# Kernel tuning notes

Measured on AMD Instinct MI355X. Metric: run time of the kernel, lower is better.

Reference implementation:

```python
import jax, jax.numpy as jnp
import numpy as np

N, B, E, D, DQ, H = 20000, 32, 320000, 128, 1024, 2
L = N // B  # 625 nodes per graph (equal-size graphs -> static max_node_num)
NUM_GNN_LAYERS = 3


def setup_inputs() -> dict:
    key = jax.random.key(0)
    ks = jax.random.split(key, 32)
    rn = lambda k, s, scale=1.0: jax.random.normal(k, s, jnp.float32) * scale
    w = lambda k, fi, fo: rn(k, (fi, fo), 1.0 / np.sqrt(fi))
    inp = {
        'x': rn(ks[0], (N, D)),
        'edge_attr': rn(ks[1], (E, D)),
        'u': rn(ks[2], (B, D)),
        'qa_attr': rn(ks[3], (B, DQ)),
        # edge MLP: cat(src,dest,edge_attr,u[eb]) = 4D -> hidden D -> D
        'W_e1': w(ks[4], 4 * D, D), 'b_e1': jnp.zeros((D,)),
        'W_e2': w(ks[5], D, D), 'b_e2': jnp.zeros((D,)),
        # weight mlp: cat(edge_attr, u[eb]) = 2D -> 1 (num_layers=1)
        'W_w': w(ks[6], 2 * D, 1), 'b_w': jnp.zeros((1,)),
        # message mlp: cat(x[row], edge_attr) = 2D -> D -> D
        'W_m1': w(ks[7], 2 * D, D), 'b_m1': jnp.zeros((D,)),
        'W_m2': w(ks[8], D, D), 'b_m2': jnp.zeros((D,)),
        # update mlp: cat(x, received, u[nb]) = 3D -> D -> D
        'W_u1': w(ks[9], 3 * D, D), 'b_u1': jnp.zeros((D,)),
        'W_u2': w(ks[10], D, D), 'b_u2': jnp.zeros((D,)),
        # multihead att-pool: q from qa_attr (DQ) -> H*dk; k,v from evidence (D) -> H*dk
        'W_q': w(ks[11], DQ, D), 'b_q': jnp.zeros((D,)),
        'W_k': w(ks[12], D, D), 'b_k': jnp.zeros((D,)),
        'W_v': w(ks[13], D, D), 'b_v': jnp.zeros((D,)),
        'edge_index': jax.random.randint(ks[14], (2, E), 0, N, dtype=jnp.int32),
        'node_batch': (jnp.arange(N, dtype=jnp.int32) // L).astype(jnp.int32),
        'num_of_nodes': jnp.full((B,), L, dtype=jnp.int32),
    }
    return inp


def _mlp2(h, W1, b1, W2, b2):
    return jax.nn.relu(h @ W1 + b1) @ W2 + b2


def _seg_softmax(logits, seg, num):
    m = jax.ops.segment_max(logits, seg, num_segments=num)
    e = jnp.exp(logits - m[seg])
    s = jax.ops.segment_sum(e, seg, num_segments=num)
    return e / s[seg]


def reference(x, edge_attr, u, qa_attr,
              W_e1, b_e1, W_e2, b_e2, W_w, b_w,
              W_m1, b_m1, W_m2, b_m2, W_u1, b_u1, W_u2, b_u2,
              W_q, b_q, W_k, b_k, W_v, b_v,
              edge_index, node_batch, num_of_nodes):
    row, col = edge_index[0], edge_index[1]
    edge_batch = node_batch[row]
    Bsz, Nn = u.shape[0], x.shape[0]
    Lm = Nn // Bsz  # static max_node_num (equal-size graphs)

    norm_w = None
    for _ in range(NUM_GNN_LAYERS):
        ue = u[edge_batch]  # [E, D]
        # EdgeModel: cat(src, dest, edge_attr, u[eb]) -> MLP -> new edge_attr
        new_edge = _mlp2(jnp.concatenate([x[row], x[col], edge_attr, ue], 1),
                         W_e1, b_e1, W_e2, b_e2)
        # edge weights from OLD edge_attr (per EdgeV1Model.forward)
        wts = jnp.concatenate([edge_attr, ue], 1) @ W_w + b_w  # [E,1]
        norm_w = _seg_softmax(wts[:, 0], edge_batch, Bsz)[:, None]  # [E,1]
        edge_attr = new_edge
        # NodeModel: message MLP, weighted scatter_mean over col, update MLP
        msg = _mlp2(jnp.concatenate([x[row], edge_attr], 1), W_m1, b_m1, W_m2, b_m2)
        summed = jax.ops.segment_sum(msg * norm_w, col, num_segments=Nn)
        cnt = jax.ops.segment_sum(jnp.ones((msg.shape[0],), msg.dtype), col, num_segments=Nn)
        received = summed / jnp.maximum(cnt, 1.0)[:, None]
        x = _mlp2(jnp.concatenate([x, received, u[node_batch]], 1),
                  W_u1, b_u1, W_u2, b_u2)

    pooled_edge = jax.ops.segment_sum(edge_attr * norm_w, edge_batch, num_segments=Bsz)  # [B,D]
    # evidence packing: equal graphs -> simple reshape, then exact GELU
    evidence = jax.nn.gelu(x.reshape(Bsz, Lm, -1), approximate=False)  # [B,L,D]
    mask = jnp.arange(Lm)[None, :] >= num_of_nodes[:, None]  # [B,L] True = masked

    # MultiheadAttPoolLayer
    dk = W_k.shape[1] // H
    q = (qa_attr @ W_q + b_q).reshape(Bsz, H, dk)
    k = (evidence @ W_k + b_k).reshape(Bsz, Lm, H, dk)
    v = (evidence @ W_v + b_v).reshape(Bsz, Lm, H, dk)
    scores = jnp.einsum('bhd,blhd->bhl', q, k) / jnp.sqrt(jnp.float32(dk))
    scores = jnp.where(mask[:, None, :], -1e30, scores)
    attn = jax.nn.softmax(scores, axis=-1)
    pooled_node = jnp.einsum('bhl,blhd->bhd', attn, v).reshape(Bsz, H * dk)  # [B,D]

    return jnp.concatenate([pooled_edge, pooled_node], 1)  # [B, 2D]
```

## Files before the change

### kernel.cpp

```cpp
#include <hip/hip_runtime.h>
#include <math.h>

typedef __bf16 bf16_t;
typedef bf16_t bf16x8 __attribute__((ext_vector_type(8)));
typedef bf16_t bf16x4 __attribute__((ext_vector_type(4)));
typedef float  f32x4  __attribute__((ext_vector_type(4)));

#define N_NODES 20000
#define NEDGE   320000
#define DIM     128
#define TP      136
#define EBLK    2500
#define FBLK    10000
#define NBLK    625

#define FE1  0
#define FE2  49152
#define FM1  65536
#define FM2  98304
#define FU1  114688
#define FU2  163840
#define FK   180224
#define FV   196608
#define WF_ELEMS 212992

__device__ __forceinline__ void acc_zero(f32x4 acc[2][8]) {
  f32x4 z = {0.f, 0.f, 0.f, 0.f};
#pragma unroll
  for (int i = 0; i < 2; ++i)
#pragma unroll
    for (int j = 0; j < 8; ++j) acc[i][j] = z;
}

__device__ __forceinline__ void wstage_rows_bf(bf16_t* sA, const bf16_t* src, int rowreg, int lane) {
  int r = lane >> 1, h = lane & 1;
  int row = __shfl(rowreg, r);
  const bf16_t* sp = src + (size_t)row * DIM + h * 64;
  bf16_t* dp = sA + r * TP + h * 64;
#pragma unroll
  for (int i = 0; i < 8; ++i)
    *(uint4*)(dp + i * 8) = *(const uint4*)(sp + i * 8);
}

__device__ __forceinline__ void wstage_rows_f32(bf16_t* sA, const float* src, int rowreg, int lane) {
  int r = lane >> 1, h = lane & 1;
  int row = __shfl(rowreg, r);
  const float* sp = src + (size_t)row * DIM + h * 64;
  bf16_t* dp = sA + r * TP + h * 64;
#pragma unroll
  for (int i = 0; i < 8; ++i) {
    float4 f0 = *(const float4*)(sp + i * 8);
    float4 f1 = *(const float4*)(sp + i * 8 + 4);
    bf16x8 tv;
    tv[0]=(bf16_t)f0.x; tv[1]=(bf16_t)f0.y; tv[2]=(bf16_t)f0.z; tv[3]=(bf16_t)f0.w;
    tv[4]=(bf16_t)f1.x; tv[5]=(bf16_t)f1.y; tv[6]=(bf16_t)f1.z; tv[7]=(bf16_t)f1.w;
    *(bf16x8*)(dp + i * 8) = tv;
  }
}

__device__ __forceinline__ void wstage_seq_bf(bf16_t* sA, const bf16_t* src, int base, int lane) {
  int r = lane >> 1, h = lane & 1;
  const bf16_t* sp = src + (size_t)(base + r) * DIM + h * 64;
  bf16_t* dp = sA + r * TP + h * 64;
#pragma unroll
  for (int i = 0; i < 8; ++i)
    *(uint4*)(dp + i * 8) = *(const uint4*)(sp + i * 8);
}

__device__ __forceinline__ void wstage_seq_f32(bf16_t* sA, const float* src, int base, int lane) {
  int r = lane >> 1, h = lane & 1;
  const float* sp = src + (size_t)(base + r) * DIM + h * 64;
  bf16_t* dp = sA + r * TP + h * 64;
#pragma unroll
  for (int i = 0; i < 8; ++i) {
    float4 f0 = *(const float4*)(sp + i * 8);
    float4 f1 = *(const float4*)(sp + i * 8 + 4);
    bf16x8 tv;
    tv[0]=(bf16_t)f0.x; tv[1]=(bf16_t)f0.y; tv[2]=(bf16_t)f0.z; tv[3]=(bf16_t)f0.w;
    tv[4]=(bf16_t)f1.x; tv[5]=(bf16_t)f1.y; tv[6]=(bf16_t)f1.z; tv[7]=(bf16_t)f1.w;
    *(bf16x8*)(dp + i * 8) = tv;
  }
}

__device__ __forceinline__ void wmfma_gk128(const bf16_t* sA, const bf16_t* __restrict__ Wf,
                                            int lane, int lm, int lq, f32x4 acc[2][8]) {
#pragma unroll
  for (int kk = 0; kk < 4; ++kk) {
    int ko = kk * 32 + lq * 8;
    bf16x8 a0 = *(const bf16x8*)(sA + lm * TP + ko);
    bf16x8 a1 = *(const bf16x8*)(sA + (16 + lm) * TP + ko);
    const bf16_t* wp = Wf + ((kk * 8) << 9) + (lane << 3);
#pragma unroll
    for (int ct = 0; ct < 8; ++ct) {
      bf16x8 bfr = *(const bf16x8*)(wp + (ct << 9));
      acc[0][ct] = __builtin_amdgcn_mfma_f32_16x16x32_bf16(a0, bfr, acc[0][ct], 0, 0, 0);
      acc[1][ct] = __builtin_amdgcn_mfma_f32_16x16x32_bf16(a1, bfr, acc[1][ct], 0, 0, 0);
    }
  }
}

__device__ __forceinline__ void merge_shfl(float& m, float& s, int width) {
  for (int k = 1; k < width; k <<= 1) {
    float m2 = __shfl_xor(m, k), s2 = __shfl_xor(s, k);
    float M = fmaxf(m, m2), ns = 0.f;
    if (m  > -1e29f) ns += s  * expf(m  - M);
    if (m2 > -1e29f) ns += s2 * expf(m2 - M);
    m = M; s = ns;
  }
}

__global__ void gn_xcvt(const float* x, bf16_t* xb) {
  int i = blockIdx.x * 256 + threadIdx.x;
  if (i < N_NODES * DIM / 4) {
    float4 f = ((const float4*)x)[i];
    bf16x4 o; o[0]=(bf16_t)f.x; o[1]=(bf16_t)f.y; o[2]=(bf16_t)f.z; o[3]=(bf16_t)f.w;
    *(bf16x4*)(xb + (size_t)i * 4) = o;
  }
}

__global__ void gn_fragw(const float* We1, const float* We2, const float* Wm1, const float* Wm2,
                         const float* Wu1, const float* Wu2, const float* Wk, const float* Wv,
                         bf16_t* WF) {
  int idx = blockIdx.x * 256 + threadIdx.x;
  if (idx >= WF_ELEMS) return;
  int seg = idx >> 14;
  const float* W; int kc;
  switch (seg) {
    case 0:  W = We1; kc = 0; break;
    case 1:  W = We1; kc = 1; break;
    case 2:  W = We1; kc = 2; break;
    case 3:  W = We2; kc = 0; break;
    case 4:  W = Wm1; kc = 0; break;
    case 5:  W = Wm1; kc = 1; break;
    case 6:  W = Wm2; kc = 0; break;
    case 7:  W = Wu1; kc = 0; break;
    case 8:  W = Wu1; kc = 1; break;
    case 9:  W = Wu1; kc = 2; break;
    case 10: W = Wu2; kc = 0; break;
    case 11: W = Wk;  kc = 0; break;
    default: W = Wv;  kc = 0; break;
  }
  int r = idx & 16383;
  int j = r & 7, lane = (r >> 3) & 63, ct = (r >> 9) & 7, kk = (r >> 12) & 3;
  int k = kc * 128 + kk * 32 + (lane >> 4) * 8 + j;
  int n = ct * 16 + (lane & 15);
  WF[idx] = (bf16_t)W[k * 128 + n];
}

__global__ void gn_uprep(const float* u, const float* We1, const float* be1,
// ... 34 lines not shown
  int t = threadIdx.x;
  int sub = t & 15, grp = t >> 4;
  for (int e = blockIdx.x * 16 + grp; e < NEDGE; e += gridDim.x * 16) {
    const float* er = ea + (size_t)e * DIM + sub * 8;
    float s = 0.f;
#pragma unroll
    for (int j = 0; j < 8; ++j) s += er[j] * Ww[sub * 8 + j];
#pragma unroll
    for (int m = 1; m < 16; m <<= 1) s += __shfl_xor(s, m);
    if (sub == 0) {
      int g = nbat[ei[e]];
      wl[e] = s + uw[g];
      gb[e] = g;
    }
  }
}

__global__ void gn_part0(const float* wl, const int* gb, float* pm, float* ps) {
  __shared__ float lv[128];
  __shared__ int   lgg[128];
  int t = threadIdx.x, blk = blockIdx.x, e0 = blk * 128;
  if (t < 128) { lv[t] = wl[e0 + t]; lgg[t] = gb[e0 + t]; }
  __syncthreads();
  int g = t >> 3, seg = t & 7;
  float m = -1e30f, s = 0.f;
  for (int i = seg * 16; i < seg * 16 + 16; ++i)
    if (lgg[i] == g) {
      float v = lv[i];
      if (v > m) { s = s * expf(m - v) + 1.f; m = v; }
      else s += expf(v - m);
    }
  merge_shfl(m, s, 8);
  if (seg == 0) { pm[blk * 32 + g] = m; ps[blk * 32 + g] = s; }
}

__global__ void gn_reduce_ms(const float* pm, const float* ps, float* mg, float* sg, int nb) {
  int g = blockIdx.x, t = threadIdx.x;
  __shared__ float red[256];
  float m = -1e30f;
  for (int i = t; i < nb; i += 256) m = fmaxf(m, pm[i * 32 + g]);
  red[t] = m; __syncthreads();
  for (int s2 = 128; s2 > 0; s2 >>= 1) { if (t < s2) red[t] = fmaxf(red[t], red[t + s2]); __syncthreads(); }
  m = red[0]; __syncthreads();
  float s = 0.f;
  for (int i = t; i < nb; i += 256) {
    float sb = ps[i * 32 + g];
    if (sb > 0.f) s += sb * expf(pm[i * 32 + g] - m);
  }
  red[t] = s; __syncthreads();
  for (int s2 = 128; s2 > 0; s2 >>= 1) { if (t < s2) red[t] += red[t + s2]; __syncthreads(); }
  if (t == 0) { mg[g] = m; sg[g] = red[0]; }
}

__global__ __launch_bounds__(64, 2) void gn_fused(
    const bf16_t* __restrict__ xb,
    const void* esrcv, int efirst,
    bf16_t* edst,
    const bf16_t* __restrict__ WF,
    const float* R, const float* UW, const float* Wwv,
    const float* be2, const float* bm1, const float* bm2,
    const float* wl_cur, const float* mg, const float* sg,
    float* wl_next, float* pm, float* ps, int last,
    const int* ei, const int* gb, float* recv) {
  __shared__ bf16_t sA[32 * TP];
  __shared__ float slwt[32];

  int lane = threadIdx.x;
  int blk = blockIdx.x;
  int e0 = blk * 32;
  int lm = lane & 15, lq = lane >> 4;

  int lrowr = 0, lcolr = 0, lgr = 0;
  float lnwr = 0.f;
  if (lane < 32) {
    int e = e0 + lane;
    lrowr = ei[e];
    lcolr = ei[NEDGE + e];
    int g = gb[e];
    lgr = g;
    lnwr = expf(wl_cur[e] - mg[g]) / sg[g];
  }

  f32x4 accE[2][8], accM[2][8];
  acc_zero(accE);
  acc_zero(accM);

  wstage_rows_bf(sA, xb, lrowr, lane);
  wmfma_gk128(sA, WF + FE1, lane, lm, lq, accE);
  wmfma_gk128(sA, WF + FM1, lane, lm, lq, accM);
  wstage_rows_bf(sA, xb, lcolr, lane);
  wmfma_gk128(sA, WF + FE1 + 16384, lane, lm, lq, accE);
  if (efirst) wstage_seq_f32(sA, (const float*)esrcv, e0, lane);
  else        wstage_seq_bf (sA, (const bf16_t*)esrcv, e0, lane);
  wmfma_gk128(sA, WF + FE1 + 32768, lane, lm, lq, accE);

#pragma unroll
  for (int rt = 0; rt < 2; ++rt)
#pragma unroll
    for (int reg = 0; reg < 4; ++reg) {
      int row = rt * 16 + lq * 4 + reg;
      const float* Rr = R + (size_t)__shfl(lgr, row) * DIM;
#pragma unroll
      for (int ct = 0; ct < 8; ++ct) {
        int col = ct * 16 + lm;
        sA[row * TP + col] = (bf16_t)fmaxf(accE[rt][ct][reg] + Rr[col], 0.f);
      }
    }
  acc_zero(accE);
  wmfma_gk128(sA, WF + FE2, lane, lm, lq, accE);

  {
    float ww8[8], be8[8];
#pragma unroll
    for (int ct = 0; ct < 8; ++ct) { ww8[ct] = Wwv[ct * 16 + lm]; be8[ct] = be2[ct * 16 + lm]; }
#pragma unroll
    for (int rt = 0; rt < 2; ++rt)
#pragma unroll
      for (int reg = 0; reg < 4; ++reg) {
        int row = rt * 16 + lq * 4 + reg;
        int g = __shfl(lgr, row);
        bf16_t* drow = edst + (size_t)(e0 + row) * DIM;
        float lsum = 0.f;
#pragma unroll
        for (int ct = 0; ct < 8; ++ct) {
          int col = ct * 16 + lm;
          float v = accE[rt][ct][reg] + be8[ct];
          drow[col] = (bf16_t)v;
          sA[row * TP + col] = (bf16_t)v;
          lsum += v * ww8[ct];
        }
        if (!last) {
          lsum += __shfl_xor(lsum, 1);
          lsum += __shfl_xor(lsum, 2);
          lsum += __shfl_xor(lsum, 4);
          lsum += __shfl_xor(lsum, 8);
          if (lm == 0) {
            float v2 = lsum + UW[g];
            wl_next[e0 + row] = v2;
            slwt[row] = v2;
          }
        }
      }
  }
  wmfma_gk128(sA, WF + FM1 + 16384, lane, lm, lq, accM);

  {
    float bm18[8];
#pragma unroll
    for (int ct = 0; ct < 8; ++ct) bm18[ct] = bm1[ct * 16 + lm];
#pragma unroll
    for (int rt = 0; rt < 2; ++rt)
#pragma unroll
      for (int reg = 0; reg < 4; ++reg) {
        int row = rt * 16 + lq * 4 + reg;
#pragma unroll
        for (int ct = 0; ct < 8; ++ct) {
          int col = ct * 16 + lm;
          sA[row * TP + col] = (bf16_t)fmaxf(accM[rt][ct][reg] + bm18[ct], 0.f);
        }
      }
  }
  acc_zero(accM);
  wmfma_gk128(sA, WF + FM2, lane, lm, lq, accM);

  {
    float bm28[8];
#pragma unroll
    for (int ct = 0; ct < 8; ++ct) bm28[ct] = bm2[ct * 16 + lm];
#pragma unroll
    for (int rt = 0; rt < 2; ++rt)
#pragma unroll
      for (int reg = 0; reg < 4; ++reg) {
        int row = rt * 16 + lq * 4 + reg;
        float nwv = __shfl(lnwr, row);
        float* rr = recv + (size_t)__shfl(lcolr, row) * DIM;
#pragma unroll
        for (int ct = 0; ct < 8; ++ct) {
          int col = ct * 16 + lm;
          atomicAdd(&rr[col], (accM[rt][ct][reg] + bm28[ct]) * nwv);
        }
      }
  }

  if (!last) {
    int g = lane >> 1, seg = lane & 1;
    float m = -1e30f, s = 0.f;
    for (int i = seg * 16; i < seg * 16 + 16; ++i) {
      int gi = __shfl(lgr, i);
      if (gi == g) {
        float v = slwt[i];
        if (v > m) { s = s * expf(m - v) + 1.f; m = v; }
        else s += expf(v - m);
      }
    }
    merge_shfl(m, s, 2);
    if (seg == 0) { pm[blk * 32 + g] = m; ps[blk * 32 + g] = s; }
  }
}

__global__ __launch_bounds__(64, 2) void gn_node(
    const bf16_t* xsrc, bf16_t* xdst, const float* recv, const float* cnt,
    const float* u, const bf16_t* __restrict__ WF,
    const float* bu1, const float* bu2, const int* nbat) {
  __shared__ bf16_t sA[32 * TP];

  int lane = threadIdx.x;
  int n0 = blockIdx.x * 32;
  int lm = lane & 15, lq = lane >> 4;

  int lgr = 0;
  if (lane < 32) lgr = nbat[n0 + lane];

  f32x4 acc[2][8];
  acc_zero(acc);

  wstage_seq_bf(sA, xsrc, n0, lane);
  wmfma_gk128(sA, WF + FU1, lane, lm, lq, acc);
  {
    int r = lane >> 1, h = lane & 1;
    const float* rr = recv + (size_t)(n0 + r) * DIM + h * 64;
    float ic = 1.f / fmaxf(cnt[n0 + r], 1.f);
    bf16_t* dp = sA + r * TP + h * 64;
#pragma unroll
    for (int i = 0; i < 8; ++i) {
      float4 f0 = *(const float4*)(rr + i * 8);
      float4 f1 = *(const float4*)(rr + i * 8 + 4);
      bf16x8 tv;
      tv[0]=(bf16_t)(f0.x*ic); tv[1]=(bf16_t)(f0.y*ic); tv[2]=(bf16_t)(f0.z*ic); tv[3]=(bf16_t)(f0.w*ic);
      tv[4]=(bf16_t)(f1.x*ic); tv[5]=(bf16_t)(f1.y*ic); tv[6]=(bf16_t)(f1.z*ic); tv[7]=(bf16_t)(f1.w*ic);
      *(bf16x8*)(dp + i * 8) = tv;
    }
  }
  wmfma_gk128(sA, WF + FU1 + 16384, lane, lm, lq, acc);
  wstage_rows_f32(sA, u, lgr, lane);
  wmfma_gk128(sA, WF + FU1 + 32768, lane, lm, lq, acc);

  {
    float bu18[8];
#pragma unroll
    for (int ct = 0; ct < 8; ++ct) bu18[ct] = bu1[ct * 16 + lm];
#pragma unroll
    for (int rt = 0; rt < 2; ++rt)
#pragma unroll
      for (int reg = 0; reg < 4; ++reg) {
        int row = rt * 16 + lq * 4 + reg;
#pragma unroll
        for (int ct = 0; ct < 8; ++ct) {
          int col = ct * 16 + lm;
          sA[row * TP + col] = (bf16_t)fmaxf(acc[rt][ct][reg] + bu18[ct], 0.f);
        }
      }
  }
  acc_zero(acc);
  wmfma_gk128(sA, WF + FU2, lane, lm, lq, acc);

  {
    float bu28[8];
#pragma unroll
    for (int ct = 0; ct < 8; ++ct) bu28[ct] = bu2[ct * 16 + lm];
#pragma unroll
    for (int rt = 0; rt < 2; ++rt)
#pragma unroll
      for (int reg = 0; reg < 4; ++reg) {
        int row = rt * 16 + lq * 4 + reg;
        bf16_t* dr = xdst + (size_t)(n0 + row) * DIM;
#pragma unroll
        for (int ct = 0; ct < 8; ++ct) {
          int col = ct * 16 + lm;
          dr[col] = (bf16_t)(acc[rt][ct][reg] + bu28[ct]);
        }
      }
  }
}

__global__ __launch_bounds__(64, 2) void gn_ev(
    const bf16_t* xsrc, const bf16_t* __restrict__ WF,
    const float* bk, const float* bv, float* kb, float* vb) {
  __shared__ bf16_t sA[32 * TP];

  int lane = threadIdx.x;
  int n0 = blockIdx.x * 32;
  int sel = blockIdx.y;
  const bf16_t* Wf = WF + (sel ? FV : FK);
  const float* bias = sel ? bv : bk;
  float* dst = sel ? vb : kb;
  int lm = lane & 15, lq = lane >> 4;

  {
    int r = lane >> 1, h = lane & 1;
    const bf16_t* sp = xsrc + (size_t)(n0 + r) * DIM + h * 64;
    bf16_t* dp = sA + r * TP + h * 64;
#pragma unroll
    for (int i = 0; i < 8; ++i) {
      uint4 v = *(const uint4*)(sp + i * 8);
      bf16_t tmp[8];
      *(uint4*)tmp = v;
      bf16x8 tv;
#pragma unroll
      for (int j = 0; j < 8; ++j) {
        float f = (float)tmp[j];
        tv[j] = (bf16_t)(0.5f * f * (1.f + erff(f * 0.70710678118654752f)));
      }
      *(bf16x8*)(dp + i * 8) = tv;
    }
  }

  f32x4 acc[2][8];
  acc_zero(acc);
  wmfma_gk128(sA, Wf, lane, lm, lq, acc);

  {
    float b8[8];
#pragma unroll
    for (int ct = 0; ct < 8; ++ct) b8[ct] = bias[ct * 16 + lm];
#pragma unroll
    for (int rt = 0; rt < 2; ++rt)
#pragma unroll
      for (int reg = 0; reg < 4; ++reg) {
        int row = rt * 16 + lq * 4 + reg;
        float* dr = dst + (size_t)(n0 + row) * DIM;
#pragma unroll
        for (int ct = 0; ct < 8; ++ct) {
          int col = ct * 16 + lm;
          dr[col] = acc[rt][ct][reg] + b8[ct];
        }
      }
  }
}

__global__ void gn_pooled_edge(const bf16_t* eb, const float* wl, const float* mg, const float* sg,
                               const int* gb, float* pe) {
  __shared__ float loc[4096];
  int t = threadIdx.x;
  for (int i = t; i < 4096; i += 256) loc[i] = 0.f;
  __syncthreads();
  int lane = t & 63, w = t >> 6;
  int wid = blockIdx.x * 4 + w, nw = gridDim.x * 4;
  for (int e = wid; e < NEDGE; e += nw) {
    int g = gb[e];
    float nwt = expf(wl[e] - mg[g]) / sg[g];
    const bf16_t* er = eb + (size_t)e * DIM + lane * 2;
    atomicAdd(&loc[g * 128 + lane * 2],     (float)er[0] * nwt);
    atomicAdd(&loc[g * 128 + lane * 2 + 1], (float)er[1] * nwt);
  }
  __syncthreads();
  for (int i = t; i < 4096; i += 256) atomicAdd(&pe[i], loc[i]);
}

__global__ void gn_att(const float* qb, const float* kb, const float* vb, const int* non, float* out) {
  int b = blockIdx.x >> 1, h = blockIdx.x & 1, t = threadIdx.x;
  __shared__ float qv[64];
  __shared__ float sc[625];
  __shared__ float red[256];
  if (t < 64) qv[t] = qb[b * 128 + h * 64 + t];
  __syncthreads();
  int nn = non[b];
  for (int l = t; l < 625; l += 256) {
    float acc = 0.f;
    const float* kr = kb + ((size_t)(b * 625 + l)) * DIM + h * 64;
    for (int d2 = 0; d2 < 64; ++d2) acc += qv[d2] * kr[d2];
    sc[l] = (l < nn) ? acc * 0.125f : -1e30f;
// ... 20 lines not shown
  }
}

__global__ void gn_fin(const float* pe, float* out) {
  int t = threadIdx.x;
  for (int i = t; i < 4096; i += 256) {
    int b = i >> 7, c = i & 127;
    out[b * 256 + c] = pe[i];
  }
}

extern "C" void kernel_launch(void* const* d_in, const int* in_sizes, int n_in,
                              void* d_out, int out_size, void* d_ws, size_t ws_size,
                              hipStream_t stream) {
  const float* x   = (const float*)d_in[0];
  const float* ea  = (const float*)d_in[1];
  const float* u   = (const float*)d_in[2];
  const float* qa  = (const float*)d_in[3];
  const float* We1 = (const float*)d_in[4];
  const float* be1 = (const float*)d_in[5];
  const float* We2 = (const float*)d_in[6];
  const float* be2 = (const float*)d_in[7];
  const float* Ww  = (const float*)d_in[8];
  const float* bw  = (const float*)d_in[9];
  const float* Wm1 = (const float*)d_in[10];
  const float* bm1 = (const float*)d_in[11];
  const float* Wm2 = (const float*)d_in[12];
  const float* bm2 = (const float*)d_in[13];
  const float* Wu1 = (const float*)d_in[14];
  const float* bu1 = (const float*)d_in[15];
  const float* Wu2 = (const float*)d_in[16];
  const float* bu2 = (const float*)d_in[17];
  const float* Wq  = (const float*)d_in[18];
  const float* bq  = (const float*)d_in[19];
  const float* Wk  = (const float*)d_in[20];
  const float* bk  = (const float*)d_in[21];
  const float* Wv  = (const float*)d_in[22];
  const float* bv  = (const float*)d_in[23];
  const int* ei   = (const int*)d_in[24];
  const int* nbat = (const int*)d_in[25];
  const int* non  = (const int*)d_in[26];
  float* out = (float*)d_out;

  char* p = (char*)d_ws;
  auto alloc = [&](size_t bytes) { char* r = p; p += (bytes + 255) & ~(size_t)255; return r; };
  bf16_t* EB  = (bf16_t*)alloc((size_t)NEDGE * DIM * 2);
  bf16_t* XB  = (bf16_t*)alloc((size_t)N_NODES * DIM * 2);
  bf16_t* XB0 = (bf16_t*)alloc((size_t)N_NODES * DIM * 2);
  float* RECV = (float*)alloc((size_t)N_NODES * DIM * 4);
  float* CNT  = (float*)alloc((size_t)N_NODES * 4);
  float* WL   = (float*)alloc((size_t)NEDGE * 4);
  float* WLn  = (float*)alloc((size_t)NEDGE * 4);
  int*   GB   = (int*)alloc((size_t)NEDGE * 4);
  float* PM   = (float*)alloc((size_t)FBLK * 32 * 4);
  float* PS   = (float*)alloc((size_t)FBLK * 32 * 4);
  float* MG   = (float*)alloc(32 * 4);
  float* SG   = (float*)alloc(32 * 4);
  float* R    = (float*)alloc(32 * 128 * 4);
  float* UW   = (float*)alloc(32 * 4);
  bf16_t* WF  = (bf16_t*)alloc((size_t)WF_ELEMS * 2);
  float* QB   = (float*)alloc(32 * 128 * 4);
  float* KB   = (float*)alloc((size_t)N_NODES * DIM * 4);
  float* VB   = (float*)alloc((size_t)N_NODES * DIM * 4);
  float* PE   = (float*)alloc(32 * 128 * 4);

  hipMemsetAsync(CNT, 0, (size_t)N_NODES * 4, stream);
  hipMemsetAsync(PE, 0, 32 * 128 * 4, stream);

  gn_xcvt<<<(N_NODES * DIM / 4 + 255) / 256, 256, 0, stream>>>(x, XB0);
  gn_fragw<<<(WF_ELEMS + 255) / 256, 256, 0, stream>>>(We1, We2, Wm1, Wm2, Wu1, Wu2, Wk, Wv, WF);
  gn_uprep<<<16, 256, 0, stream>>>(u, We1, be1, Ww, bw, R, UW);
  gn_count<<<1250, 256, 0, stream>>>(ei, CNT);
  gn_q<<<32, 256, 0, stream>>>(qa, Wq, bq, QB);
  gn_wl0<<<2500, 256, 0, stream>>>(ea, Ww, UW, ei, nbat, WL, GB);
  gn_part0<<<EBLK, 256, 0, stream>>>(WL, GB, PM, PS);

  for (int layer = 0; layer < 3; ++layer) {
    int first = (layer == 0) ? 1 : 0;
    int last = (layer == 2) ? 1 : 0;
    const bf16_t* xs = first ? XB0 : XB;
    const void* es = first ? (const void*)ea : (const void*)EB;
    float* cur = (layer == 1) ? WLn : WL;
    float* nxt = (layer == 1) ? WL : WLn;
    gn_reduce_ms<<<32, 256, 0, stream>>>(PM, PS, MG, SG, first ? EBLK : FBLK);
    hipMemsetAsync(RECV, 0, (size_t)N_NODES * DIM * 4, stream);
    gn_fused<<<FBLK, 64, 0, stream>>>(xs, es, first, EB, WF, R, UW, Ww,
                                      be2, bm1, bm2, cur, MG, SG,
                                      nxt, PM, PS, last, ei, GB, RECV);
    gn_node<<<NBLK, 64, 0, stream>>>(xs, XB, RECV, CNT, u, WF, bu1, bu2, nbat);
  }

  gn_pooled_edge<<<256, 256, 0, stream>>>(EB, WL, MG, SG, GB, PE);
  gn_ev<<<dim3(NBLK, 2), 64, 0, stream>>>(XB, WF, bk, bv, KB, VB);
  gn_att<<<64, 256, 0, stream>>>(QB, KB, VB, non, out);
  gn_fin<<<1, 256, 0, stream>>>(PE, out);
}
```

Before: 1.559 ms.

## Process 64 edges per wave and precompute node-update partial GEMM in edge kernel

The fused edge kernel now handles 64 edges per wavefront instead of 32, so each weight fragment load feeds four MFMA row tiles rather than two. This halves the block count and the per-edge-block partial softmax stats. The message MLP's x[row] term is restaged afterwards instead of kept in a second accumulator, which bounds register use. Extra blocks appended to the same launch precompute the x and u parts of the update MLP's first layer into a new PRE buffer, leaving gn_node only the received-message GEMM. The costs are a larger accumulator array and more register pressure per wave, an extra staging pass for x[row], and extra global traffic to write and read PRE.

After: 1.725 ms. 1.11x slower.

```diff
diff --git a/kernel.cpp b/kernel.cpp
--- a/kernel.cpp
+++ b/kernel.cpp
@@ -11,7 +11,7 @@
 #define DIM     128
 #define TP      136
 #define EBLK    2500
-#define FBLK    10000
+#define FBLK2   5000
 #define NBLK    625
 
 #define FE1  0
@@ -24,7 +24,7 @@
 #define FV   196608
 #define WF_ELEMS 212992
 
-__device__ __forceinline__ void acc_zero(f32x4 acc[2][8]) {
+__device__ __forceinline__ void acc_zero32(f32x4 acc[2][8]) {
   f32x4 z = {0.f, 0.f, 0.f, 0.f};
 #pragma unroll
   for (int i = 0; i < 2; ++i)
@@ -32,14 +32,14 @@
     for (int j = 0; j < 8; ++j) acc[i][j] = z;
 }
 
-__device__ __forceinline__ void wstage_rows_bf(bf16_t* sA, const bf16_t* src, int rowreg, int lane) {
-  int r = lane >> 1, h = lane & 1;
-  int row = __shfl(rowreg, r);
-  const bf16_t* sp = src + (size_t)row * DIM + h * 64;
-  bf16_t* dp = sA + r * TP + h * 64;
-#pragma unroll
-  for (int i = 0; i < 8; ++i)
-    *(uint4*)(dp + i * 8) = *(const uint4*)(sp + i * 8);
+__device__ __forceinline__ void acc_zero64(f32x4 acc[2][2][8]) {
+  f32x4 z = {0.f, 0.f, 0.f, 0.f};
+#pragma unroll
+  for (int t = 0; t < 2; ++t)
+#pragma unroll
+    for (int i = 0; i < 2; ++i)
+#pragma unroll
+      for (int j = 0; j < 8; ++j) acc[t][i][j] = z;
 }
 
 __device__ __forceinline__ void wstage_rows_f32(bf16_t* sA, const float* src, int rowreg, int lane) {
@@ -67,18 +67,49 @@
     *(uint4*)(dp + i * 8) = *(const uint4*)(sp + i * 8);
 }
 
-__device__ __forceinline__ void wstage_seq_f32(bf16_t* sA, const float* src, int base, int lane) {
-  int r = lane >> 1, h = lane & 1;
-  const float* sp = src + (size_t)(base + r) * DIM + h * 64;
-  bf16_t* dp = sA + r * TP + h * 64;
-#pragma unroll
-  for (int i = 0; i < 8; ++i) {
-    float4 f0 = *(const float4*)(sp + i * 8);
-    float4 f1 = *(const float4*)(sp + i * 8 + 4);
-    bf16x8 tv;
-    tv[0]=(bf16_t)f0.x; tv[1]=(bf16_t)f0.y; tv[2]=(bf16_t)f0.z; tv[3]=(bf16_t)f0.w;
-    tv[4]=(bf16_t)f1.x; tv[5]=(bf16_t)f1.y; tv[6]=(bf16_t)f1.z; tv[7]=(bf16_t)f1.w;
-    *(bf16x8*)(dp + i * 8) = tv;
+__device__ __forceinline__ void wstage64_rows_bf(bf16_t* band, const bf16_t* src, int rowreg, int lane) {
+  int h = lane & 1;
+#pragma unroll
+  for (int sub = 0; sub < 2; ++sub) {
+    int r = sub * 32 + (lane >> 1);
+    int row = __shfl(rowreg, r);
+    const bf16_t* sp = src + (size_t)row * DIM + h * 64;
+    bf16_t* dp = band + r * TP + h * 64;
+#pragma unroll
+    for (int i = 0; i < 8; ++i)
+      *(uint4*)(dp + i * 8) = *(const uint4*)(sp + i * 8);
+  }
+}
+
+__device__ __forceinline__ void wstage64_seq_bf(bf16_t* band, const bf16_t* src, int base, int lane) {
+  int h = lane & 1;
+#pragma unroll
+  for (int sub = 0; sub < 2; ++sub) {
+    int r = sub * 32 + (lane >> 1);
+    const bf16_t* sp = src + (size_t)(base + r) * DIM + h * 64;
+    bf16_t* dp = band + r * TP + h * 64;
+#pragma unroll
+    for (int i = 0; i < 8; ++i)
+      *(uint4*)(dp + i * 8) = *(const uint4*)(sp + i * 8);
+  }
+}
+
+__device__ __forceinline__ void wstage64_seq_f32(bf16_t* band, const float* src, int base, int lane) {
+  int h = lane & 1;
+#pragma unroll
+  for (int sub = 0; sub < 2; ++sub) {
+    int r = sub * 32 + (lane >> 1);
+    const float* sp = src + (size_t)(base + r) * DIM + h * 64;
+    bf16_t* dp = band + r * TP + h * 64;
+#pragma unroll
+    for (int i = 0; i < 8; ++i) {
+      float4 f0 = *(const float4*)(sp + i * 8);
+      float4 f1 = *(const float4*)(sp + i * 8 + 4);
+      bf16x8 tv;
+      tv[0]=(bf16_t)f0.x; tv[1]=(bf16_t)f0.y; tv[2]=(bf16_t)f0.z; tv[3]=(bf16_t)f0.w;
+      tv[4]=(bf16_t)f1.x; tv[5]=(bf16_t)f1.y; tv[6]=(bf16_t)f1.z; tv[7]=(bf16_t)f1.w;
+      *(bf16x8*)(dp + i * 8) = tv;
+    }
   }
 }
 
@@ -95,6 +126,27 @@
       bf16x8 bfr = *(const bf16x8*)(wp + (ct << 9));
       acc[0][ct] = __builtin_amdgcn_mfma_f32_16x16x32_bf16(a0, bfr, acc[0][ct], 0, 0, 0);
       acc[1][ct] = __builtin_amdgcn_mfma_f32_16x16x32_bf16(a1, bfr, acc[1][ct], 0, 0, 0);
+    }
+  }
+}
+
+__device__ __forceinline__ void wmfma64(const bf16_t* band, const bf16_t* __restrict__ Wf,
+                                        int lane, int lm, int lq, f32x4 acc[2][2][8]) {
+#pragma unroll
+  for (int kk = 0; kk < 4; ++kk) {
+    int ko = kk * 32 + lq * 8;
+    bf16x8 a0 = *(const bf16x8*)(band + lm * TP + ko);
+    bf16x8 a1 = *(const bf16x8*)(band + (16 + lm) * TP + ko);
+    bf16x8 a2 = *(const bf16x8*)(band + (32 + lm) * TP + ko);
+    bf16x8 a3 = *(const bf16x8*)(band + (48 + lm) * TP + ko);
+    const bf16_t* wp = Wf + ((kk * 8) << 9) + (lane << 3);
+#pragma unroll
+    for (int ct = 0; ct < 8; ++ct) {
+      bf16x8 bfr = *(const bf16x8*)(wp + (ct << 9));
+      acc[0][0][ct] = __builtin_amdgcn_mfma_f32_16x16x32_bf16(a0, bfr, acc[0][0][ct], 0, 0, 0);
+      acc[0][1][ct] = __builtin_amdgcn_mfma_f32_16x16x32_bf16(a1, bfr, acc[0][1][ct], 0, 0, 0);
+      acc[1][0][ct] = __builtin_amdgcn_mfma_f32_16x16x32_bf16(a2, bfr, acc[1][0][ct], 0, 0, 0);
+      acc[1][1][ct] = __builtin_amdgcn_mfma_f32_16x16x32_bf16(a3, bfr, acc[1][1][ct], 0, 0, 0);
     }
   }
 }
@@ -244,131 +296,158 @@
     const float* be2, const float* bm1, const float* bm2,
     const float* wl_cur, const float* mg, const float* sg,
     float* wl_next, float* pm, float* ps, int last,
-    const int* ei, const int* gb, float* recv) {
-  __shared__ bf16_t sA[32 * TP];
-  __shared__ float slwt[32];
+    const int* ei, const int* gb, float* recv,
+    const float* uu, const float* bu1, const int* nbat, float* pre) {
+  __shared__ bf16_t sS[64 * TP];
+  __shared__ float slwt[64];
 
   int lane = threadIdx.x;
+  int lm = lane & 15, lq = lane >> 4;
   int blk = blockIdx.x;
-  int e0 = blk * 32;
-  int lm = lane & 15, lq = lane >> 4;
-
-  int lrowr = 0, lcolr = 0, lgr = 0;
-  float lnwr = 0.f;
-  if (lane < 32) {
-    int e = e0 + lane;
-    lrowr = ei[e];
-    lcolr = ei[NEDGE + e];
-    int g = gb[e];
-    lgr = g;
-    lnwr = expf(wl_cur[e] - mg[g]) / sg[g];
-  }
-
-  f32x4 accE[2][8], accM[2][8];
-  acc_zero(accE);
-  acc_zero(accM);
-
-  wstage_rows_bf(sA, xb, lrowr, lane);
-  wmfma_gk128(sA, WF + FE1, lane, lm, lq, accE);
-  wmfma_gk128(sA, WF + FM1, lane, lm, lq, accM);
-  wstage_rows_bf(sA, xb, lcolr, lane);
-  wmfma_gk128(sA, WF + FE1 + 16384, lane, lm, lq, accE);
-  if (efirst) wstage_seq_f32(sA, (const float*)esrcv, e0, lane);
-  else        wstage_seq_bf (sA, (const bf16_t*)esrcv, e0, lane);
-  wmfma_gk128(sA, WF + FE1 + 32768, lane, lm, lq, accE);
-
-#pragma unroll
-  for (int rt = 0; rt < 2; ++rt)
-#pragma unroll
-    for (int reg = 0; reg < 4; ++reg) {
-      int row = rt * 16 + lq * 4 + reg;
-      const float* Rr = R + (size_t)__shfl(lgr, row) * DIM;
-#pragma unroll
-      for (int ct = 0; ct < 8; ++ct) {
-        int col = ct * 16 + lm;
-        sA[row * TP + col] = (bf16_t)fmaxf(accE[rt][ct][reg] + Rr[col], 0.f);
+
+  if (blk >= FBLK2) {
+    int nb = blk - FBLK2;
+    int n0 = nb * 32;
+    int lgr = 0;
+    if (lane < 32) lgr = nbat[n0 + lane];
+    f32x4 acc[2][8];
+    acc_zero32(acc);
+    wstage_seq_bf(sS, xb, n0, lane);
+    wmfma_gk128(sS, WF + FU1, lane, lm, lq, acc);
+    wstage_rows_f32(sS, uu, lgr, lane);
+    wmfma_gk128(sS, WF + FU1 + 32768, lane, lm, lq, acc);
+    float* pp = pre + (size_t)nb * 4096 + lane * 64;
+#pragma unroll
+    for (int rt = 0; rt < 2; ++rt)
+#pragma unroll
+      for (int reg = 0; reg < 4; ++reg)
+#pragma unroll
+        for (int ct = 0; ct < 8; ++ct)
+          pp[rt * 32 + reg * 8 + ct] = acc[rt][ct][reg] + bu1[ct * 16 + lm];
+    return;
+  }
+
+  int e0 = blk * 64;
+  int lrowr = ei[e0 + lane];
+  int lcolr = ei[NEDGE + e0 + lane];
+  int lgr = gb[e0 + lane];
+  float lnwr = expf(wl_cur[e0 + lane] - mg[lgr]) / sg[lgr];
+
+  f32x4 acc[2][2][8];
+  acc_zero64(acc);
+
+  wstage64_rows_bf(sS, xb, lrowr, lane);
+  wmfma64(sS, WF + FE1, lane, lm, lq, acc);
+  wstage64_rows_bf(sS, xb, lcolr, lane);
+  wmfma64(sS, WF + FE1 + 16384, lane, lm, lq, acc);
+  if (efirst) wstage64_seq_f32(sS, (const float*)esrcv, e0, lane);
+  else        wstage64_seq_bf (sS, (const bf16_t*)esrcv, e0, lane);
+  wmfma64(sS, WF + FE1 + 32768, lane, lm, lq, acc);
+
+#pragma unroll
+  for (int tile = 0; tile < 2; ++tile)
+#pragma unroll
+    for (int rt = 0; rt < 2; ++rt)
+#pragma unroll
+      for (int reg = 0; reg < 4; ++reg) {
+        int row = tile * 32 + rt * 16 + lq * 4 + reg;
+        const float* Rr = R + (size_t)__shfl(lgr, row) * DIM;
+#pragma unroll
+        for (int ct = 0; ct < 8; ++ct) {
+          int col = ct * 16 + lm;
+          sS[row * TP + col] = (bf16_t)fmaxf(acc[tile][rt][ct][reg] + Rr[col], 0.f);
+        }
       }
-    }
-  acc_zero(accE);
-  wmfma_gk128(sA, WF + FE2, lane, lm, lq, accE);
+  acc_zero64(acc);
+  wmfma64(sS, WF + FE2, lane, lm, lq, acc);
 
   {
     float ww8[8], be8[8];
 #pragma unroll
     for (int ct = 0; ct < 8; ++ct) { ww8[ct] = Wwv[ct * 16 + lm]; be8[ct] = be2[ct * 16 + lm]; }
 #pragma unroll
-    for (int rt = 0; rt < 2; ++rt)
-#pragma unroll
-      for (int reg = 0; reg < 4; ++reg) {
-        int row = rt * 16 + lq * 4 + reg;
-        int g = __shfl(lgr, row);
-        bf16_t* drow = edst + (size_t)(e0 + row) * DIM;
-        float lsum = 0.f;
-#pragma unroll
-        for (int ct = 0; ct < 8; ++ct) {
-          int col = ct * 16 + lm;
-          float v = accE[rt][ct][reg] + be8[ct];
-          drow[col] = (bf16_t)v;
-          sA[row * TP + col] = (bf16_t)v;
-          lsum += v * ww8[ct];
-        }
-        if (!last) {
-          lsum += __shfl_xor(lsum, 1);
-          lsum += __shfl_xor(lsum, 2);
-          lsum += __shfl_xor(lsum, 4);
-          lsum += __shfl_xor(lsum, 8);
-          if (lm == 0) {
-            float v2 = lsum + UW[g];
-            wl_next[e0 + row] = v2;
-            slwt[row] = v2;
+    for (int tile = 0; tile < 2; ++tile)
+#pragma unroll
+      for (int rt = 0; rt < 2; ++rt)
+#pragma unroll
+        for (int reg = 0; reg < 4; ++reg) {
+          int row = tile * 32 + rt * 16 + lq * 4 + reg;
+          int g = __shfl(lgr, row);
+          bf16_t* drow = edst + (size_t)(e0 + row) * DIM;
+          float lsum = 0.f;
+#pragma unroll
+          for (int ct = 0; ct < 8; ++ct) {
+            int col = ct * 16 + lm;
+            float v = acc[tile][rt][ct][reg] + be8[ct];
+            drow[col] = (bf16_t)v;
+            sS[row * TP + col] = (bf16_t)v;
+            lsum += v * ww8[ct];
+          }
+          if (!last) {
+            lsum += __shfl_xor(lsum, 1);
+            lsum += __shfl_xor(lsum, 2);
+            lsum += __shfl_xor(lsum, 4);
+            lsum += __shfl_xor(lsum, 8);
+            if (lm == 0) {
+              float v2 = lsum + UW[g];
+              wl_next[e0 + row] = v2;
+              slwt[row] = v2;
+            }
           }
         }
-      }
-  }
-  wmfma_gk128(sA, WF + FM1 + 16384, lane, lm, lq, accM);
+  }
+
+  acc_zero64(acc);
+  wmfma64(sS, WF + FM1 + 16384, lane, lm, lq, acc);
+  wstage64_rows_bf(sS, xb, lrowr, lane);
+  wmfma64(sS, WF + FM1, lane, lm, lq, acc);
 
   {
     float bm18[8];
 #pragma unroll
     for (int ct = 0; ct < 8; ++ct) bm18[ct] = bm1[ct * 16 + lm];
 #pragma unroll
-    for (int rt = 0; rt < 2; ++rt)
-#pragma unroll
-      for (int reg = 0; reg < 4; ++reg) {
-        int row = rt * 16 + lq * 4 + reg;
-#pragma unroll
-        for (int ct = 0; ct < 8; ++ct) {
-          int col = ct * 16 + lm;
-          sA[row * TP + col] = (bf16_t)fmaxf(accM[rt][ct][reg] + bm18[ct], 0.f);
+    for (int tile = 0; tile < 2; ++tile)
+#pragma unroll
+      for (int rt = 0; rt < 2; ++rt)
+#pragma unroll
+        for (int reg = 0; reg < 4; ++reg) {
+          int row = tile * 32 + rt * 16 + lq * 4 + reg;
+#pragma unroll
+          for (int ct = 0; ct < 8; ++ct) {
+            int col = ct * 16 + lm;
+            sS[row * TP + col] = (bf16_t)fmaxf(acc[tile][rt][ct][reg] + bm18[ct], 0.f);
+          }
         }
-      }
-  }
-  acc_zero(accM);
-  wmfma_gk128(sA, WF + FM2, lane, lm, lq, accM);
+  }
+  acc_zero64(acc);
+  wmfma64(sS, WF + FM2, lane, lm, lq, acc);
 
   {
     float bm28[8];
 #pragma unroll
     for (int ct = 0; ct < 8; ++ct) bm28[ct] = bm2[ct * 16 + lm];
 #pragma unroll
-    for (int rt = 0; rt < 2; ++rt)
-#pragma unroll
-      for (int reg = 0; reg < 4; ++reg) {
-        int row = rt * 16 + lq * 4 + reg;
-        float nwv = __shfl(lnwr, row);
-        float* rr = recv + (size_t)__shfl(lcolr, row) * DIM;
-#pragma unroll
-        for (int ct = 0; ct < 8; ++ct) {
-          int col = ct * 16 + lm;
-          atomicAdd(&rr[col], (accM[rt][ct][reg] + bm28[ct]) * nwv);
+    for (int tile = 0; tile < 2; ++tile)
+#pragma unroll
+      for (int rt = 0; rt < 2; ++rt)
+#pragma unroll
+        for (int reg = 0; reg < 4; ++reg) {
+          int row = tile * 32 + rt * 16 + lq * 4 + reg;
+          float nwv = __shfl(lnwr, row);
+          float* rr = recv + (size_t)__shfl(lcolr, row) * DIM;
+#pragma unroll
+          for (int ct = 0; ct < 8; ++ct) {
+            int col = ct * 16 + lm;
+            atomicAdd(&rr[col], (acc[tile][rt][ct][reg] + bm28[ct]) * nwv);
+          }
         }
-      }
   }
 
   if (!last) {
     int g = lane >> 1, seg = lane & 1;
     float m = -1e30f, s = 0.f;
-    for (int i = seg * 16; i < seg * 16 + 16; ++i) {
+    for (int i = seg * 32; i < seg * 32 + 32; ++i) {
       int gi = __shfl(lgr, i);
       if (gi == g) {
         float v = slwt[i];
@@ -382,23 +461,15 @@
 }
 
 __global__ __launch_bounds__(64, 2) void gn_node(
-    const bf16_t* xsrc, bf16_t* xdst, const float* recv, const float* cnt,
-    const float* u, const bf16_t* __restrict__ WF,
-    const float* bu1, const float* bu2, const int* nbat) {
+    bf16_t* xdst, const float* recv, const float* cnt, const float* pre,
+    const bf16_t* __restrict__ WF, const float* bu2) {
   __shared__ bf16_t sA[32 * TP];
 
   int lane = threadIdx.x;
-  int n0 = blockIdx.x * 32;
+  int nb = blockIdx.x;
+  int n0 = nb * 32;
   int lm = lane & 15, lq = lane >> 4;
 
-  int lgr = 0;
-  if (lane < 32) lgr = nbat[n0 + lane];
-
-  f32x4 acc[2][8];
-  acc_zero(acc);
-
-  wstage_seq_bf(sA, xsrc, n0, lane);
-  wmfma_gk128(sA, WF + FU1, lane, lm, lq, acc);
   {
     int r = lane >> 1, h = lane & 1;
     const float* rr = recv + (size_t)(n0 + r) * DIM + h * 64;
@@ -414,27 +485,24 @@
       *(bf16x8*)(dp + i * 8) = tv;
     }
   }
+
+  f32x4 acc[2][8];
+  acc_zero32(acc);
   wmfma_gk128(sA, WF + FU1 + 16384, lane, lm, lq, acc);
-  wstage_rows_f32(sA, u, lgr, lane);
-  wmfma_gk128(sA, WF + FU1 + 32768, lane, lm, lq, acc);
-
-  {
-    float bu18[8];
-#pragma unroll
-    for (int ct = 0; ct < 8; ++ct) bu18[ct] = bu1[ct * 16 + lm];
-#pragma unroll
-    for (int rt = 0; rt < 2; ++rt)
-#pragma unroll
-      for (int reg = 0; reg < 4; ++reg) {
-        int row = rt * 16 + lq * 4 + reg;
-#pragma unroll
-        for (int ct = 0; ct < 8; ++ct) {
-          int col = ct * 16 + lm;
-          sA[row * TP + col] = (bf16_t)fmaxf(acc[rt][ct][reg] + bu18[ct], 0.f);
-        }
+
+  const float* pp = pre + (size_t)nb * 4096 + lane * 64;
+#pragma unroll
+  for (int rt = 0; rt < 2; ++rt)
+#pragma unroll
+    for (int reg = 0; reg < 4; ++reg) {
+      int row = rt * 16 + lq * 4 + reg;
+#pragma unroll
+      for (int ct = 0; ct < 8; ++ct) {
+        int col = ct * 16 + lm;
+        sA[row * TP + col] = (bf16_t)fmaxf(acc[rt][ct][reg] + pp[rt * 32 + reg * 8 + ct], 0.f);
       }
-  }
-  acc_zero(acc);
+    }
+  acc_zero32(acc);
   wmfma_gk128(sA, WF + FU2, lane, lm, lq, acc);
 
   {
@@ -489,7 +557,7 @@
   }
 
   f32x4 acc[2][8];
-  acc_zero(acc);
+  acc_zero32(acc);
   wmfma_gk128(sA, Wf, lane, lm, lq, acc);
 
   {
@@ -616,8 +684,8 @@
   float* WL   = (float*)alloc((size_t)NEDGE * 4);
   float* WLn  = (float*)alloc((size_t)NEDGE * 4);
   int*   GB   = (int*)alloc((size_t)NEDGE * 4);
-  float* PM   = (float*)alloc((size_t)FBLK * 32 * 4);
-  float* PS   = (float*)alloc((size_t)FBLK * 32 * 4);
+  float* PM   = (float*)alloc((size_t)FBLK2 * 32 * 4);
+  float* PS   = (float*)alloc((size_t)FBLK2 * 32 * 4);
   float* MG   = (float*)alloc(32 * 4);
   float* SG   = (float*)alloc(32 * 4);
   float* R    = (float*)alloc(32 * 128 * 4);
@@ -627,6 +695,7 @@
   float* KB   = (float*)alloc((size_t)N_NODES * DIM * 4);
   float* VB   = (float*)alloc((size_t)N_NODES * DIM * 4);
   float* PE   = (float*)alloc(32 * 128 * 4);
+  float* PRE  = (float*)alloc((size_t)N_NODES * DIM * 4);
 
   hipMemsetAsync(CNT, 0, (size_t)N_NODES * 4, stream);
   hipMemsetAsync(PE, 0, 32 * 128 * 4, stream);
@@ -646,12 +715,13 @@
     const void* es = first ? (const void*)ea : (const void*)EB;
     float* cur = (layer == 1) ? WLn : WL;
     float* nxt = (layer == 1) ? WL : WLn;
-    gn_reduce_ms<<<32, 256, 0, stream>>>(PM, PS, MG, SG, first ? EBLK : FBLK);
+    gn_reduce_ms<<<32, 256, 0, stream>>>(PM, PS, MG, SG, first ? EBLK : FBLK2);
     hipMemsetAsync(RECV, 0, (size_t)N_NODES * DIM * 4, stream);
-    gn_fused<<<FBLK, 64, 0, stream>>>(xs, es, first, EB, WF, R, UW, Ww,
-                                      be2, bm1, bm2, cur, MG, SG,
-                                      nxt, PM, PS, last, ei, GB, RECV);
-    gn_node<<<NBLK, 64, 0, stream>>>(xs, XB, RECV, CNT, u, WF, bu1, bu2, nbat);
+    gn_fused<<<FBLK2 + NBLK, 64, 0, stream>>>(xs, es, first, EB, WF, R, UW, Ww,
+                                              be2, bm1, bm2, cur, MG, SG,
+                                              nxt, PM, PS, last, ei, GB, RECV,
+                                              u, bu1, nbat, PRE);
+    gn_node<<<NBLK, 64, 0, stream>>>(XB, RECV, CNT, PRE, WF, bu2);
   }
 
   gn_pooled_edge<<<256, 256, 0, stream>>>(EB, WL, MG, SG, GB, PE);
```

## Split fused edge/message kernel into two kernels and precompute node-update partials

Applied to the files above, without the earlier changes.

The fused edge+message kernel, which held two accumulator sets, is split into gn_edge and gn_msg, each holding a single accumulator set. This lowers register pressure, and launch bounds rise from 2 to 3 blocks per SM. The message kernel re-stages x[row] and reads the new edge features back from global memory. Extra blocks in gn_msg precompute the x and u parts of the node update into a PRE buffer, leaving gn_node less work. The cost is an extra launch, re-gathering x rows, and extra global traffic for the edge features and PRE.

Result: slower. 1.849 ms (+18.6%).

```diff
diff --git a/kernel.cpp b/kernel.cpp
--- a/kernel.cpp
+++ b/kernel.cpp
@@ -24,7 +24,7 @@
 #define FV   196608
 #define WF_ELEMS 212992
 
-__device__ __forceinline__ void acc_zero(f32x4 acc[2][8]) {
+__device__ __forceinline__ void acc_zero32(f32x4 acc[2][8]) {
   f32x4 z = {0.f, 0.f, 0.f, 0.f};
 #pragma unroll
   for (int i = 0; i < 2; ++i)
@@ -235,16 +235,14 @@
   if (t == 0) { mg[g] = m; sg[g] = red[0]; }
 }
 
-__global__ __launch_bounds__(64, 2) void gn_fused(
+__global__ __launch_bounds__(64, 3) void gn_edge(
     const bf16_t* __restrict__ xb,
     const void* esrcv, int efirst,
     bf16_t* edst,
     const bf16_t* __restrict__ WF,
-    const float* R, const float* UW, const float* Wwv,
-    const float* be2, const float* bm1, const float* bm2,
-    const float* wl_cur, const float* mg, const float* sg,
+    const float* R, const float* UW, const float* Wwv, const float* be2,
     float* wl_next, float* pm, float* ps, int last,
-    const int* ei, const int* gb, float* recv) {
+    const int* ei, const int* gb) {
   __shared__ bf16_t sA[32 * TP];
   __shared__ float slwt[32];
 
@@ -254,28 +252,23 @@
   int lm = lane & 15, lq = lane >> 4;
 
   int lrowr = 0, lcolr = 0, lgr = 0;
-  float lnwr = 0.f;
   if (lane < 32) {
     int e = e0 + lane;
     lrowr = ei[e];
     lcolr = ei[NEDGE + e];
-    int g = gb[e];
-    lgr = g;
-    lnwr = expf(wl_cur[e] - mg[g]) / sg[g];
-  }
-
-  f32x4 accE[2][8], accM[2][8];
-  acc_zero(accE);
-  acc_zero(accM);
+    lgr = gb[e];
+  }
+
+  f32x4 acc[2][8];
+  acc_zero32(acc);
 
   wstage_rows_bf(sA, xb, lrowr, lane);
-  wmfma_gk128(sA, WF + FE1, lane, lm, lq, accE);
-  wmfma_gk128(sA, WF + FM1, lane, lm, lq, accM);
+  wmfma_gk128(sA, WF + FE1, lane, lm, lq, acc);
   wstage_rows_bf(sA, xb, lcolr, lane);
-  wmfma_gk128(sA, WF + FE1 + 16384, lane, lm, lq, accE);
+  wmfma_gk128(sA, WF + FE1 + 16384, lane, lm, lq, acc);
   if (efirst) wstage_seq_f32(sA, (const float*)esrcv, e0, lane);
   else        wstage_seq_bf (sA, (const bf16_t*)esrcv, e0, lane);
-  wmfma_gk128(sA, WF + FE1 + 32768, lane, lm, lq, accE);
+  wmfma_gk128(sA, WF + FE1 + 32768, lane, lm, lq, acc);
 
 #pragma unroll
   for (int rt = 0; rt < 2; ++rt)
@@ -286,11 +279,11 @@
 #pragma unroll
       for (int ct = 0; ct < 8; ++ct) {
         int col = ct * 16 + lm;
-        sA[row * TP + col] = (bf16_t)fmaxf(accE[rt][ct][reg] + Rr[col], 0.f);
-      }
-    }
-  acc_zero(accE);
-  wmfma_gk128(sA, WF + FE2, lane, lm, lq, accE);
+        sA[row * TP + col] = (bf16_t)fmaxf(acc[rt][ct][reg] + Rr[col], 0.f);
+      }
+    }
+  acc_zero32(acc);
+  wmfma_gk128(sA, WF + FE2, lane, lm, lq, acc);
 
   {
     float ww8[8], be8[8];
@@ -307,9 +300,8 @@
 #pragma unroll
         for (int ct = 0; ct < 8; ++ct) {
           int col = ct * 16 + lm;
-          float v = accE[rt][ct][reg] + be8[ct];
+          float v = acc[rt][ct][reg] + be8[ct];
           drow[col] = (bf16_t)v;
-          sA[row * TP + col] = (bf16_t)v;
           lsum += v * ww8[ct];
         }
         if (!last) {
@@ -325,45 +317,6 @@
         }
       }
   }
-  wmfma_gk128(sA, WF + FM1 + 16384, lane, lm, lq, accM);
-
-  {
-    float bm18[8];
-#pragma unroll
-    for (int ct = 0; ct < 8; ++ct) bm18[ct] = bm1[ct * 16 + lm];
-#pragma unroll
-    for (int rt = 0; rt < 2; ++rt)
-#pragma unroll
-      for (int reg = 0; reg < 4; ++reg) {
-        int row = rt * 16 + lq * 4 + reg;
-#pragma unroll
-        for (int ct = 0; ct < 8; ++ct) {
-          int col = ct * 16 + lm;
-          sA[row * TP + col] = (bf16_t)fmaxf(accM[rt][ct][reg] + bm18[ct], 0.f);
-        }
-      }
-  }
-  acc_zero(accM);
-  wmfma_gk128(sA, WF + FM2, lane, lm, lq, accM);
-
-  {
-    float bm28[8];
-#pragma unroll
-    for (int ct = 0; ct < 8; ++ct) bm28[ct] = bm2[ct * 16 + lm];
-#pragma unroll
-    for (int rt = 0; rt < 2; ++rt)
-#pragma unroll
-      for (int reg = 0; reg < 4; ++reg) {
-        int row = rt * 16 + lq * 4 + reg;
-        float nwv = __shfl(lnwr, row);
-        float* rr = recv + (size_t)__shfl(lcolr, row) * DIM;
-#pragma unroll
-        for (int ct = 0; ct < 8; ++ct) {
-          int col = ct * 16 + lm;
-          atomicAdd(&rr[col], (accM[rt][ct][reg] + bm28[ct]) * nwv);
-        }
-      }
-  }
 
   if (!last) {
     int g = lane >> 1, seg = lane & 1;
@@ -381,24 +334,110 @@
   }
 }
 
-__global__ __launch_bounds__(64, 2) void gn_node(
-    const bf16_t* xsrc, bf16_t* xdst, const float* recv, const float* cnt,
-    const float* u, const bf16_t* __restrict__ WF,
-    const float* bu1, const float* bu2, const int* nbat) {
+__global__ __launch_bounds__(64, 3) void gn_msg(
+    const bf16_t* __restrict__ xb,
+    const bf16_t* __restrict__ eb,
+    const bf16_t* __restrict__ WF,
+    const float* bm1, const float* bm2,
+    const float* wl_cur, const float* mg, const float* sg,
+    const int* ei, const int* gb, float* recv,
+    const float* uu, const float* bu1, const int* nbat, float* pre) {
   __shared__ bf16_t sA[32 * TP];
 
   int lane = threadIdx.x;
-  int n0 = blockIdx.x * 32;
   int lm = lane & 15, lq = lane >> 4;
-
-  int lgr = 0;
-  if (lane < 32) lgr = nbat[n0 + lane];
+  int blk = blockIdx.x;
+
+  if (blk >= FBLK) {
+    int nb = blk - FBLK;
+    int n0 = nb * 32;
+    int lgr = 0;
+    if (lane < 32) lgr = nbat[n0 + lane];
+    f32x4 acc[2][8];
+    acc_zero32(acc);
+    wstage_seq_bf(sA, xb, n0, lane);
+    wmfma_gk128(sA, WF + FU1, lane, lm, lq, acc);
+    wstage_rows_f32(sA, uu, lgr, lane);
+    wmfma_gk128(sA, WF + FU1 + 32768, lane, lm, lq, acc);
+    float* pp = pre + (size_t)nb * 4096 + lane * 64;
+#pragma unroll
+    for (int rt = 0; rt < 2; ++rt)
+#pragma unroll
+      for (int reg = 0; reg < 4; ++reg)
+#pragma unroll
+        for (int ct = 0; ct < 8; ++ct)
+          pp[rt * 32 + reg * 8 + ct] = acc[rt][ct][reg] + bu1[ct * 16 + lm];
+    return;
+  }
+
+  int e0 = blk * 32;
+  int lrowr = 0, lcolr = 0;
+  float lnwr = 0.f;
+  if (lane < 32) {
+    int e = e0 + lane;
+    lrowr = ei[e];
+    lcolr = ei[NEDGE + e];
+    int g = gb[e];
+    lnwr = expf(wl_cur[e] - mg[g]) / sg[g];
+  }
 
   f32x4 acc[2][8];
-  acc_zero(acc);
-
-  wstage_seq_bf(sA, xsrc, n0, lane);
-  wmfma_gk128(sA, WF + FU1, lane, lm, lq, acc);
+  acc_zero32(acc);
+
+  wstage_rows_bf(sA, xb, lrowr, lane);
+  wmfma_gk128(sA, WF + FM1, lane, lm, lq, acc);
+  wstage_seq_bf(sA, eb, e0, lane);
+  wmfma_gk128(sA, WF + FM1 + 16384, lane, lm, lq, acc);
+
+  {
+    float bm18[8];
+#pragma unroll
+    for (int ct = 0; ct < 8; ++ct) bm18[ct] = bm1[ct * 16 + lm];
+#pragma unroll
+    for (int rt = 0; rt < 2; ++rt)
+#pragma unroll
+      for (int reg = 0; reg < 4; ++reg) {
+        int row = rt * 16 + lq * 4 + reg;
+#pragma unroll
+        for (int ct = 0; ct < 8; ++ct) {
+          int col = ct * 16 + lm;
+          sA[row * TP + col] = (bf16_t)fmaxf(acc[rt][ct][reg] + bm18[ct], 0.f);
+        }
+      }
+  }
+  acc_zero32(acc);
+  wmfma_gk128(sA, WF + FM2, lane, lm, lq, acc);
+
+  {
+    float bm28[8];
+#pragma unroll
+    for (int ct = 0; ct < 8; ++ct) bm28[ct] = bm2[ct * 16 + lm];
+#pragma unroll
+    for (int rt = 0; rt < 2; ++rt)
+#pragma unroll
+      for (int reg = 0; reg < 4; ++reg) {
+        int row = rt * 16 + lq * 4 + reg;
+        float nwv = __shfl(lnwr, row);
+        float* rr = recv + (size_t)__shfl(lcolr, row) * DIM;
+#pragma unroll
+        for (int ct = 0; ct < 8; ++ct) {
+          int col = ct * 16 + lm;
+          atomicAdd(&rr[col], (acc[rt][ct][reg] + bm28[ct]) * nwv);
+        }
+      }
+  }
+}
+
+__global__ __launch_bounds__(64, 3) void gn_node(
+    bf16_t* xdst, const float* recv, const float* cnt, const float* pre,
+    const bf16_t* __restrict__ WF, const float* bu2) {
+  __shared__ bf16_t sA[32 * TP];
+
+  int lane = threadIdx.x;
+  int nb = blockIdx.x;
+  int n0 = nb * 32;
+  int lm = lane & 15, lq = lane >> 4;
+
   {
     int r = lane >> 1, h = lane & 1;
     const float* rr = recv + (size_t)(n0 + r) * DIM + h * 64;
@@ -414,27 +453,24 @@
       *(bf16x8*)(dp + i * 8) = tv;
     }
   }
+
+  f32x4 acc[2][8];
+  acc_zero32(acc);
   wmfma_gk128(sA, WF + FU1 + 16384, lane, lm, lq, acc);
-  wstage_rows_f32(sA, u, lgr, lane);
-  wmfma_gk128(sA, WF + FU1 + 32768, lane, lm, lq, acc);
-
-  {
-    float bu18[8];
-#pragma unroll
-    for (int ct = 0; ct < 8; ++ct) bu18[ct] = bu1[ct * 16 + lm];
-#pragma unroll
-    for (int rt = 0; rt < 2; ++rt)
-#pragma unroll
-      for (int reg = 0; reg < 4; ++reg) {
-        int row = rt * 16 + lq * 4 + reg;
-#pragma unroll
-        for (int ct = 0; ct < 8; ++ct) {
-          int col = ct * 16 + lm;
-          sA[row * TP + col] = (bf16_t)fmaxf(acc[rt][ct][reg] + bu18[ct], 0.f);
-        }
-      }
-  }
-  acc_zero(acc);
+
+  const float* pp = pre + (size_t)nb * 4096 + lane * 64;
+#pragma unroll
+  for (int rt = 0; rt < 2; ++rt)
+#pragma unroll
+    for (int reg = 0; reg < 4; ++reg) {
+      int row = rt * 16 + lq * 4 + reg;
+#pragma unroll
+      for (int ct = 0; ct < 8; ++ct) {
+        int col = ct * 16 + lm;
+        sA[row * TP + col] = (bf16_t)fmaxf(acc[rt][ct][reg] + pp[rt * 32 + reg * 8 + ct], 0.f);
+      }
+    }
+  acc_zero32(acc);
   wmfma_gk128(sA, WF + FU2, lane, lm, lq, acc);
 
   {
@@ -456,7 +492,7 @@
   }
 }
 
-__global__ __launch_bounds__(64, 2) void gn_ev(
+__global__ __launch_bounds__(64, 3) void gn_ev(
     const bf16_t* xsrc, const bf16_t* __restrict__ WF,
     const float* bk, const float* bv, float* kb, float* vb) {
   __shared__ bf16_t sA[32 * TP];
@@ -489,7 +525,7 @@
   }
 
   f32x4 acc[2][8];
-  acc_zero(acc);
+  acc_zero32(acc);
   wmfma_gk128(sA, Wf, lane, lm, lq, acc);
 
   {
@@ -627,6 +663,7 @@
   float* KB   = (float*)alloc((size_t)N_NODES * DIM * 4);
   float* VB   = (float*)alloc((size_t)N_NODES * DIM * 4);
   float* PE   = (float*)alloc(32 * 128 * 4);
+  float* PRE  = (float*)alloc((size_t)N_NODES * DIM * 4);
 
   hipMemsetAsync(CNT, 0, (size_t)N_NODES * 4, stream);
   hipMemsetAsync(PE, 0, 32 * 128 * 4, stream);
@@ -648,10 +685,11 @@
     float* nxt = (layer == 1) ? WL : WLn;
     gn_reduce_ms<<<32, 256, 0, stream>>>(PM, PS, MG, SG, first ? EBLK : FBLK);
     hipMemsetAsync(RECV, 0, (size_t)N_NODES * DIM * 4, stream);
-    gn_fused<<<FBLK, 64, 0, stream>>>(xs, es, first, EB, WF, R, UW, Ww,
-                                      be2, bm1, bm2, cur, MG, SG,
-                                      nxt, PM, PS, last, ei, GB, RECV);
-    gn_node<<<NBLK, 64, 0, stream>>>(xs, XB, RECV, CNT, u, WF, bu1, bu2, nbat);
+    gn_edge<<<FBLK, 64, 0, stream>>>(xs, es, first, EB, WF, R, UW, Ww, be2,
+                                     nxt, PM, PS, last, ei, GB);
+    gn_msg<<<FBLK + NBLK, 64, 0, stream>>>(xs, EB, WF, bm1, bm2, cur, MG, SG,
+                                           ei, GB, RECV, u, bu1, nbat, PRE);
+    gn_node<<<NBLK, 64, 0, stream>>>(XB, RECV, CNT, PRE, WF, bu2);
   }
 
   gn_pooled_edge<<<256, 256, 0, stream>>>(EB, WL, MG, SG, GB, PE);
```
